# Kernel tuning notes

Hardware: AMD Instinct MI355X
Metric: run time of the kernel (lower is better)

## Reference

```python
import jax, jax.numpy as jnp
import numpy as np

N = 50000        # nodes
E = 800000       # directed edges (before self-loops)
NODE_DIM = 128
HIDDEN = 64
HEADS = 4
C = HIDDEN // HEADS   # 16 per-head channels
LAYERS = 4
G = 256          # graphs in batch
EPS = 1e-5       # BatchNorm eps
SLOPE = 0.2      # GAT leaky_relu negative slope


def setup_inputs() -> dict:
    key = jax.random.key(0)
    ks = jax.random.split(key, 12)

    def gl(k, shape, fan_in):  # glorot-ish init
        return jax.random.normal(k, shape, jnp.float32) * np.float32(1.0 / np.sqrt(fan_in))

    x = jax.random.normal(ks[0], (N, NODE_DIM), jnp.float32)
    edge_index = jax.random.randint(ks[1], (2, E), 0, N)
    batch = jnp.sort(jax.random.randint(ks[2], (N,), 0, G))

    return {
        "x": x,
        "embed_W": gl(ks[3], (NODE_DIM, HIDDEN), NODE_DIM),
        "embed_b": jnp.zeros((HIDDEN,), jnp.float32),
        "gat_W": gl(ks[4], (LAYERS, HIDDEN, HIDDEN), HIDDEN),
        "att_src": gl(ks[5], (LAYERS, HEADS, C), C),
        "att_dst": gl(ks[6], (LAYERS, HEADS, C), C),
        "gat_b": jnp.zeros((LAYERS, HIDDEN), jnp.float32),
        "bn_gamma": jnp.ones((LAYERS, HIDDEN), jnp.float32),
        "bn_beta": jnp.zeros((LAYERS, HIDDEN), jnp.float32),
        "fc1_W": gl(ks[7], (HIDDEN, HIDDEN), HIDDEN),
        "fc1_b": jnp.zeros((HIDDEN,), jnp.float32),
        "fc2_W": gl(ks[8], (HIDDEN, 1), HIDDEN),
        "fc2_b": jnp.zeros((1,), jnp.float32),
        "edge_index": edge_index,
        "batch": batch,
    }


def reference(x, embed_W, embed_b, gat_W, att_src, att_dst, gat_b,
              bn_gamma, bn_beta, fc1_W, fc1_b, fc2_W, fc2_b,
              edge_index, batch):
    # GATConv default: add self-loops (message flows src -> dst)
    loops = jnp.arange(N)
    src = jnp.concatenate([edge_index[0], loops])
    dst = jnp.concatenate([edge_index[1], loops])

    h = x @ embed_W + embed_b  # [N, HIDDEN]
    for l in range(LAYERS):
        xp = (h @ gat_W[l]).reshape(N, HEADS, C)          # per-head transform
        a_s = jnp.sum(xp * att_src[l], axis=-1)           # [N, H]
        a_d = jnp.sum(xp * att_dst[l], axis=-1)           # [N, H]
        e = jax.nn.leaky_relu(a_s[src] + a_d[dst], SLOPE) # [E', H]
        # segment softmax over incoming edges of each dst node
        m = jax.ops.segment_max(e, dst, num_segments=N)
        p = jnp.exp(e - m[dst])
        s = jax.ops.segment_sum(p, dst, num_segments=N)
        alpha = p / (s[dst] + 1e-16)                      # [E', H]
        msg = xp[src] * alpha[:, :, None]                 # [E', H, C]
        h = jax.ops.segment_sum(msg, dst, num_segments=N).reshape(N, HIDDEN) + gat_b[l]
        # BatchNorm over nodes (training-mode batch stats, biased variance)
        mu = jnp.mean(h, axis=0)
        var = jnp.var(h, axis=0)
        h = (h - mu) * jax.lax.rsqrt(var + EPS) * bn_gamma[l] + bn_beta[l]
        h = jax.nn.elu(h)

    g = jax.ops.segment_sum(h, batch, num_segments=G)     # global_add_pool
    g = jax.nn.relu(g @ fc1_W + fc1_b)                    # dropout: identity (eval)
    return (g @ fc2_W + fc2_b).reshape(-1)                # [G]
```

## Files before the change

### kernel.cpp

```cpp
#include <hip/hip_runtime.h>

#define N_NODES 50000
#define N_EDGES 800000
#define NODE_DIM 128
#define HIDDEN 64
#define HEADS 4
#define LAYERS 4
#define NGRAPH 256
#define BN_EPS 1e-5f
#define SLOPE 0.2f
#define NTILES 196
#define BN_BLOCKS 256
#define NPW 16

typedef unsigned short u16;
typedef unsigned int   u32;

__device__ __forceinline__ float b2f(u16 v) { return __uint_as_float(((u32)v) << 16); }
__device__ __forceinline__ u16 f2b(float f) {
    u32 u = __float_as_uint(f);
    u32 r = (u + 0x7FFFu + ((u >> 16) & 1u)) >> 16;
    return (u16)r;
}
__device__ __forceinline__ float ld(const void* p, int i, int isf) {
    return isf ? ((const float*)p)[i] : b2f(((const u16*)p)[i]);
}
__device__ __forceinline__ float bcast(float v, int l) {
    return __uint_as_float((u32)__builtin_amdgcn_readlane((int)__float_as_uint(v), l));
}

__global__ void k_mark(u16* out, u16 pat) { out[threadIdx.x] = pat; }

__global__ void k_init(const void* gamma, int* flag, int* cnt) {
    int i = blockIdx.x * 256 + threadIdx.x;
    if (i < N_NODES) cnt[i] = 0;
    if (i == 0) *flag = (((const u32*)gamma)[0] == 0x3F800000u) ? 1 : 0;
}

__global__ void k_count(const int* __restrict__ ei, int* __restrict__ cnt,
                        int* __restrict__ eslot) {
    int e = blockIdx.x * 256 + threadIdx.x;
    if (e >= N_EDGES) return;
    eslot[e] = atomicAdd(&cnt[ei[N_EDGES + e]], 1);
}
__global__ void k_scan1(const int* __restrict__ cnt, int* __restrict__ row_ptr,
                        int* __restrict__ tsum) {
    int b = blockIdx.x, t = threadIdx.x, i = b * 256 + t;
    int c = (i < N_NODES) ? cnt[i] : 0;
    __shared__ int ps[256];
    ps[t] = c;
    __syncthreads();
    for (int off = 1; off < 256; off <<= 1) {
        int v = (t >= off) ? ps[t - off] : 0;
        __syncthreads();
        ps[t] += v;
        __syncthreads();
    }
    if (i < N_NODES) row_ptr[i] = ps[t] - c;
    if (t == 255) tsum[b] = ps[255];
}
__global__ void k_scan3(int* __restrict__ row_ptr, const int* __restrict__ tsum) {
    __shared__ int ps[256];
    int t = threadIdx.x;
    int c = (t < NTILES) ? tsum[t] : 0;
    ps[t] = c;
    __syncthreads();
    for (int off = 1; off < 256; off <<= 1) {
        int v = (t >= off) ? ps[t - off] : 0;
        __syncthreads();
        ps[t] += v;
        __syncthreads();
    }
    int toff_b = (blockIdx.x == 0) ? 0 : ps[blockIdx.x - 1];
    int i = blockIdx.x * 256 + t;
    if (i < N_NODES) row_ptr[i] += toff_b;
    if (i == 0) row_ptr[N_NODES] = N_EDGES;
}
__global__ void k_fill(const int* __restrict__ ei, const int* __restrict__ row_ptr,
                       const int* __restrict__ eslot, int* __restrict__ col) {
    int e = blockIdx.x * 256 + threadIdx.x;
    if (e >= N_EDGES) return;
    col[row_ptr[ei[N_EDGES + e]] + eslot[e]] = ei[e];
}

template<int ISF>
__device__ __forceinline__ float2 ldx2(const void* x, int n, int t) {
    if (ISF) {
        return ((const float2*)x)[(size_t)n * (NODE_DIM / 2) + t];
    } else {
        u32 v = ((const u32*)x)[(size_t)n * (NODE_DIM / 2) + t];
        return make_float2(__uint_as_float(v << 16), __uint_as_float(v & 0xFFFF0000u));
    }
}

template<int ISF>
__device__ __forceinline__ void embed_tr_body(const void* __restrict__ x,
                                              const void* __restrict__ W,
                                              const void* __restrict__ b,
                                              const void* __restrict__ W0,
                                              const void* __restrict__ asrc,
                                              const void* __restrict__ adst,
                                              u16* __restrict__ xp16,
                                              float* __restrict__ a_s,
                                              float* __restrict__ a_d,
                                              float* __restrict__ bn_part) {
    int t = threadIdx.x;
    int n0 = blockIdx.x * NPW;
    if (blockIdx.x < BN_BLOCKS) {
        bn_part[blockIdx.x * 128 + t] = 0.f;
        bn_part[blockIdx.x * 128 + 64 + t] = 0.f;
    }
    float wreg[NODE_DIM];
#pragma unroll
    for (int k = 0; k < NODE_DIM; k++) wreg[k] = ld(W, k * HIDDEN + t, ISF);
    float w0[HIDDEN];
#pragma unroll
    for (int k = 0; k < HIDDEN; k++) w0[k] = ld(W0, k * HIDDEN + t, ISF);
    float bias = ld(b, t, ISF);
    float vsc = ld(asrc, t, ISF);
    float vdc = ld(adst, t, ISF);

    float2 r[4], rn[4];
#pragma unroll
    for (int i = 0; i < 4; i++) r[i] = ldx2<ISF>(x, n0 + i, t);

    for (int g = 0; g < NPW / 4; g++) {
        if (g + 1 < NPW / 4) {
#pragma unroll
            for (int i = 0; i < 4; i++) rn[i] = ldx2<ISF>(x, n0 + (g + 1) * 4 + i, t);
        }
#pragma unroll
        for (int i = 0; i < 4; i++) {
            int n = n0 + g * 4 + i;
            float a0 = 0.f, a1 = 0.f, a2 = 0.f, a3 = 0.f;
#pragma unroll
            for (int j = 0; j < 64; j += 2) {
                a0 = fmaf(bcast(r[i].x, j),     wreg[2 * j],     a0);
                a1 = fmaf(bcast(r[i].y, j),     wreg[2 * j + 1], a1);
                a2 = fmaf(bcast(r[i].x, j + 1), wreg[2 * j + 2], a2);
                a3 = fmaf(bcast(r[i].y, j + 1), wreg[2 * j + 3], a3);
            }
            float hv = (a0 + a1) + (a2 + a3) + bias;
            float c0 = 0.f, c1 = 0.f, c2 = 0.f, c3 = 0.f;
#pragma unroll
            for (int j = 0; j < HIDDEN; j += 4) {
                c0 = fmaf(bcast(hv, j),     w0[j],     c0);
                c1 = fmaf(bcast(hv, j + 1), w0[j + 1], c1);
                c2 = fmaf(bcast(hv, j + 2), w0[j + 2], c2);
                c3 = fmaf(bcast(hv, j + 3), w0[j + 3], c3);
            }
            float acc = (c0 + c1) + (c2 + c3);
            xp16[(size_t)n * HIDDEN + t] = f2b(acc);
            float vs = acc * vsc, vd = acc * vdc;
#pragma unroll
            for (int o = 1; o < 16; o <<= 1) {
                vs += __shfl_xor(vs, o, 16);
                vd += __shfl_xor(vd, o, 16);
            }
            if ((t & 15) == 0) {
                a_s[n * HEADS + (t >> 4)] = vs;
                a_d[n * HEADS + (t >> 4)] = vd;
            }
        }
#pragma unroll
        for (int i = 0; i < 4; i++) r[i] = rn[i];
    }
}
__global__ void __launch_bounds__(64)
k_embed_tr(const void* __restrict__ x, const void* __restrict__ W,
           const void* __restrict__ b, const void* __restrict__ W0,
           const void* __restrict__ asrc, const void* __restrict__ adst,
           const int* __restrict__ fl,
           u16* __restrict__ xp16, float* __restrict__ a_s, float* __restrict__ a_d,
           float* __restrict__ bn_part) {
    if (*fl) embed_tr_body<1>(x, W, b, W0, asrc, adst, xp16, a_s, a_d, bn_part);
    else     embed_tr_body<0>(x, W, b, W0, asrc, adst, xp16, a_s, a_d, bn_part);
}

template<int ISF>
__device__ __forceinline__ void transform_body(const float* __restrict__ h,
                                               const void* __restrict__ W,
                                               const void* __restrict__ asrc,
                                               const void* __restrict__ adst, int l,
                                               const float* __restrict__ bnss,
                                               u16* __restrict__ xp16,
                                               float* __restrict__ a_s,
                                               float* __restrict__ a_d,
                                               float* __restrict__ bn_part) {
    int t = threadIdx.x;
    int n0 = blockIdx.x * NPW;
    if (blockIdx.x < BN_BLOCKS) {
        bn_part[blockIdx.x * 128 + t] = 0.f;
        bn_part[blockIdx.x * 128 + 64 + t] = 0.f;
    }
    float wreg[HIDDEN];
#pragma unroll
    for (int k = 0; k < HIDDEN; k++) wreg[k] = ld(W, l * HIDDEN * HIDDEN + k * HIDDEN + t, ISF);
    float vsc = ld(asrc, l * HIDDEN + t, ISF);
    float vdc = ld(adst, l * HIDDEN + t, ISF);
    float sc = bnss[t], sh = bnss[64 + t];

    float v[4], vn[4];
#pragma unroll
    for (int i = 0; i < 4; i++) {
        float u = h[(size_t)(n0 + i) * HIDDEN + t];
        u = u * sc + sh;
        v[i] = u > 0.f ? u : (__expf(u) - 1.f);
    }

    for (int g = 0; g < NPW / 4; g++) {
        if (g + 1 < NPW / 4) {
#pragma unroll
            for (int i = 0; i < 4; i++)
                vn[i] = h[(size_t)(n0 + (g + 1) * 4 + i) * HIDDEN + t];
        }
#pragma unroll
        for (int i = 0; i < 4; i++) {
            int n = n0 + g * 4 + i;
            float c0 = 0.f, c1 = 0.f, c2 = 0.f, c3 = 0.f;
#pragma unroll
            for (int j = 0; j < HIDDEN; j += 4) {
                c0 = fmaf(bcast(v[i], j),     wreg[j],     c0);
                c1 = fmaf(bcast(v[i], j + 1), wreg[j + 1], c1);
                c2 = fmaf(bcast(v[i], j + 2), wreg[j + 2], c2);
                c3 = fmaf(bcast(v[i], j + 3), wreg[j + 3], c3);
            }
            float acc = (c0 + c1) + (c2 + c3);
            xp16[(size_t)n * HIDDEN + t] = f2b(acc);
            float vs = acc * vsc, vd = acc * vdc;
#pragma unroll
            for (int o = 1; o < 16; o <<= 1) {
                vs += __shfl_xor(vs, o, 16);
                vd += __shfl_xor(vd, o, 16);
            }
            if ((t & 15) == 0) {
                a_s[n * HEADS + (t >> 4)] = vs;
                a_d[n * HEADS + (t >> 4)] = vd;
            }
        }
        if (g + 1 < NPW / 4) {
#pragma unroll
            for (int i = 0; i < 4; i++) {
                float u = vn[i] * sc + sh;
                v[i] = u > 0.f ? u : (__expf(u) - 1.f);
            }
        }
    }
}
__global__ void __launch_bounds__(64)
k_transform(const float* __restrict__ h, const void* __restrict__ W,
            const void* __restrict__ asrc, const void* __restrict__ adst,
            const int* __restrict__ fl, int l,
            const float* __restrict__ bnss,
            u16* __restrict__ xp16, float* __restrict__ a_s,
            float* __restrict__ a_d, float* __restrict__ bn_part) {
    if (*fl) transform_body<1>(h, W, asrc, adst, l, bnss, xp16, a_s, a_d, bn_part);
    else     transform_body<0>(h, W, asrc, adst, l, bnss, xp16, a_s, a_d, bn_part);
}

__global__ void __launch_bounds__(256)
k_gather(const int* __restrict__ row_ptr, const int* __restrict__ col,
         const float* __restrict__ a_s, const float* __restrict__ a_d,
         const u16* __restrict__ xp16, float* __restrict__ h,
         float* __restrict__ bn_part) {
    int d = blockIdx.x * 4 + (threadIdx.x >> 6);
    int t = threadIdx.x & 63;
    int hd = t >> 4, l16 = t & 15, hb = hd << 4;
    int beg = row_ptr[d], end = row_ptr[d + 1];
    float ad = a_d[d * HEADS + hd];

    float m = a_s[d * HEADS + hd] + ad;
    m = m > 0.f ? m : SLOPE * m;
    float s = 1.f;
    float acc = b2f(xp16[(size_t)d * HIDDEN + t]);

    for (int j0 = beg; j0 < end; j0 += 16) {
        int jj = j0 + l16;
        int sv = col[jj < end ? jj : end - 1];
        float e = -1e30f;
        if (jj < end) {
            e = a_s[sv * HEADS + hd] + ad;
            e = e > 0.f ? e : SLOPE * e;
        }
        float cm = e;
#pragma unroll
        for (int o = 1; o < 16; o <<= 1) cm = fmaxf(cm, __shfl_xor(cm, o, 16));
        float nm = fmaxf(m, cm);
        float scale = __expf(m - nm);
        float alpha = (jj < end) ? __expf(e - nm) : 0.f;
        float cs = alpha;
#pragma unroll
        for (int o = 1; o < 16; o <<= 1) cs += __shfl_xor(cs, o, 16);
        s = s * scale + cs;
        acc *= scale;
#pragma unroll
        for (int q = 0; q < 16; q++) {
            int   svq = __shfl(sv, q, 64);
            float aq  = __shfl(alpha, hb + q, 64);
            acc += aq * b2f(xp16[(size_t)svq * HIDDEN + t]);
        }
        m = nm;
    }
    float v = acc / (s + 1e-16f);
    h[(size_t)d * HIDDEN + t] = v;

    __shared__ float s1[256];
    __shared__ float s2[256];
    s1[threadIdx.x] = v;
    s2[threadIdx.x] = v * v;
    __syncthreads();
    if (threadIdx.x < 64) {
        float su = s1[t] + s1[64 + t] + s1[128 + t] + s1[192 + t];
        float sq = s2[t] + s2[64 + t] + s2[128 + t] + s2[192 + t];
        float* bp = bn_part + (blockIdx.x & (BN_BLOCKS - 1)) * 128;
        atomicAdd(bp + t, su);
        atomicAdd(bp + 64 + t, sq);
    }
}

__global__ void k_bn_final(const float* __restrict__ bn_part,
                           const void* __restrict__ gamma, const void* __restrict__ beta,
                           const int* __restrict__ fl, int l, float* __restrict__ bnss) {
    int t = threadIdx.x;
    float sum = 0.f, sq = 0.f;
#pragma unroll 8
    for (int b = 0; b < BN_BLOCKS; b++) {
        sum += bn_part[b * 128 + t];
        sq  += bn_part[b * 128 + 64 + t];
    }
    int isf = *fl;
    const float inv_n = 1.f / (float)N_NODES;
    float mu  = sum * inv_n;
    float var = sq * inv_n - mu * mu;
    float sc = rsqrtf(var + BN_EPS) * ld(gamma, l * HIDDEN + t, isf);
    bnss[t]      = sc;
    bnss[64 + t] = ld(beta, l * HIDDEN + t, isf) - mu * sc;
}

__global__ void __launch_bounds__(1024)
k_poolmlp(const float* __restrict__ h, const int* __restrict__ batch,
          const float* __restrict__ bnss,
          const void* __restrict__ W1, const void* __restrict__ b1,
          const void* __restrict__ W2, const void* __restrict__ b2,
          const int* __restrict__ fl, void* __restrict__ out) {
    int gr = blockIdx.x;
    int t = threadIdx.x & 63, w = threadIdx.x >> 6;
    int lo = 0, hi = N_NODES;
    while (lo < hi) { int mid = (lo + hi) >> 1; if (batch[mid] < gr) lo = mid + 1; else hi = mid; }
    int beg = lo;
    lo = 0; hi = N_NODES;
    while (lo < hi) { int mid = (lo + hi) >> 1; if (batch[mid] < gr + 1) lo = mid + 1; else hi = mid; }
    int end = lo;
    float sc = bnss[t], sh = bnss[64 + t];
    float acc = 0.f;
    for (int n = beg + w; n < end; n += 16) {
        float v = h[(size_t)n * HIDDEN + t] * sc + sh;
        acc += v > 0.f ? v : (__expf(v) - 1.f);
    }
    __shared__ float sd[1024];
    __shared__ float gs[64];
    sd[threadIdx.x] = acc;
    __syncthreads();
    if (w < 8) sd[threadIdx.x] += sd[threadIdx.x + 512];
    __syncthreads();
    if (w < 4) sd[threadIdx.x] += sd[threadIdx.x + 256];
    __syncthreads();
    if (w < 2) sd[threadIdx.x] += sd[threadIdx.x + 128];
    __syncthreads();
    if (w == 0) gs[t] = sd[t] + sd[t + 64];
    __syncthreads();
    if (w == 0) {
        int isf = *fl;
        float a1 = ld(b1, t, isf);
        for (int k = 0; k < HIDDEN; k++) a1 += gs[k] * ld(W1, k * HIDDEN + t, isf);
        a1 = fmaxf(a1, 0.f);
        float p = a1 * ld(W2, t, isf);
#pragma unroll
        for (int o = 1; o < 64; o <<= 1) p += __shfl_xor(p, o, 64);
        if (t == 0) {
            float r = p + ld(b2, 0, isf);
            if (isf) ((float*)out)[gr] = r;
            else     ((u16*)out)[gr]   = f2b(r);
        }
    }
}

extern "C" void kernel_launch(void* const* d_in, const int* in_sizes, int n_in,
                              void* d_out, int out_size, void* d_ws, size_t ws_size,
                              hipStream_t stream) {
    u16* out16 = (u16*)d_out;

    bool sizes_ok = (n_in == 15) && (out_size == NGRAPH)
        && in_sizes[0] == N_NODES * NODE_DIM
        && in_sizes[1] == NODE_DIM * HIDDEN
        && in_sizes[2] == HIDDEN
        && in_sizes[3] == LAYERS * HIDDEN * HIDDEN
        && in_sizes[4] == LAYERS * HIDDEN
        && in_sizes[5] == LAYERS * HIDDEN
        && in_sizes[6] == LAYERS * HIDDEN
        && in_sizes[7] == LAYERS * HIDDEN
        && in_sizes[8] == LAYERS * HIDDEN
        && in_sizes[9] == HIDDEN * HIDDEN
        && in_sizes[10] == HIDDEN
        && in_sizes[11] == HIDDEN
        && in_sizes[12] == 1
        && in_sizes[13] == 2 * N_EDGES
        && in_sizes[14] == N_NODES;
    if (!sizes_ok) { k_mark<<<1, 256, 0, stream>>>(out16, 0x4442); return; }

    float* ws      = (float*)d_ws;
    float* h       = ws;
    u16*   xp16    = (u16*)(ws + 3200000);
    float* a_s     = ws + 4800000;
    float* a_d     = ws + 5000000;
    float* bn_part = ws + 5200000;
    float* bnss    = ws + 5232768;
    int* row_ptr   = (int*)(ws + 5232896);
    int* cnt       = row_ptr + 50001;
    int* eslot     = cnt + 50000;
    int* col       = eslot + 800000;
    int* tsum      = col + 800000;
    int* dflag     = tsum + 256;

    const size_t NEED_BYTES =
        (size_t)(5232896 + 50001 + 50000 + 800000 + 800000 + 256 + 1) * 4;
    if (ws_size < NEED_BYTES) { k_mark<<<1, 256, 0, stream>>>(out16, 0x447A); return; }

    const void* x        = d_in[0];
    const void* embed_W  = d_in[1];
    const void* embed_b  = d_in[2];
    const void* gat_W    = d_in[3];
    const void* att_src  = d_in[4];
    const void* att_dst  = d_in[5];
    const void* bn_gamma = d_in[7];
    const void* bn_beta  = d_in[8];
    const void* fc1_W    = d_in[9];
    const void* fc1_b    = d_in[10];
    const void* fc2_W    = d_in[11];
    const void* fc2_b    = d_in[12];
    const int* ei        = (const int*)d_in[13];
    const int* batch     = (const int*)d_in[14];

    const int e_blocks = (N_EDGES + 255) / 256;
    k_init<<<(N_NODES + 255) / 256, 256, 0, stream>>>(bn_gamma, dflag, cnt);
    k_count<<<e_blocks, 256, 0, stream>>>(ei, cnt, eslot);
    k_scan1<<<NTILES, 256, 0, stream>>>(cnt, row_ptr, tsum);
    k_scan3<<<NTILES, 256, 0, stream>>>(row_ptr, tsum);
    k_fill<<<e_blocks, 256, 0, stream>>>(ei, row_ptr, eslot, col);

    k_embed_tr<<<N_NODES / NPW, 64, 0, stream>>>(x, embed_W, embed_b, gat_W,
                                                 att_src, att_dst, dflag,
                                                 xp16, a_s, a_d, bn_part);

    for (int l = 0; l < LAYERS; l++) {
        if (l > 0)
            k_transform<<<N_NODES / NPW, 64, 0, stream>>>(h, gat_W, att_src, att_dst,
                                                          dflag, l, bnss,
                                                          xp16, a_s, a_d, bn_part);
        k_gather<<<N_NODES / 4, 256, 0, stream>>>(row_ptr, col, a_s, a_d, xp16, h, bn_part);
        k_bn_final<<<1, 64, 0, stream>>>(bn_part, bn_gamma, bn_beta, dflag, l, bnss);
    }

    k_poolmlp<<<NGRAPH, 1024, 0, stream>>>(h, batch, bnss, fc1_W, fc1_b, fc2_W, fc2_b,
                                           dflag, d_out);
}
```

Measured before the change: 471.0 us.

## Fold embed and first GAT weights; stage node rows in LDS for transforms

A setup kernel now precomputes embed_W·gat_W[0] and the folded bias, so the first transform is a single 128→64 matvec instead of two chained matvecs. Both transform kernels replace per-lane readlane broadcasts with per-wave double-buffered LDS rows read as float4. They also launch 256-thread blocks holding four independent waves instead of 64-thread blocks. This is meant to cut ALU and scalar-broadcast work in the dense transforms, at the cost of LDS traffic, a small extra precompute, and slightly different rounding.

```diff
diff --git a/kernel.cpp b/kernel.cpp
--- a/kernel.cpp
+++ b/kernel.cpp
@@ -12,6 +12,7 @@
 #define NTILES 196
 #define BN_BLOCKS 256
 #define NPW 16
+#define GBLK ((N_NODES + 4 * NPW - 1) / (4 * NPW))
 
 typedef unsigned short u16;
 typedef unsigned int   u32;
@@ -25,16 +26,33 @@
 __device__ __forceinline__ float ld(const void* p, int i, int isf) {
     return isf ? ((const float*)p)[i] : b2f(((const u16*)p)[i]);
 }
-__device__ __forceinline__ float bcast(float v, int l) {
-    return __uint_as_float((u32)__builtin_amdgcn_readlane((int)__float_as_uint(v), l));
-}
 
 __global__ void k_mark(u16* out, u16 pat) { out[threadIdx.x] = pat; }
 
-__global__ void k_init(const void* gamma, int* flag, int* cnt) {
-    int i = blockIdx.x * 256 + threadIdx.x;
-    if (i < N_NODES) cnt[i] = 0;
-    if (i == 0) *flag = (((const u32*)gamma)[0] == 0x3F800000u) ? 1 : 0;
+__global__ void k_initw(const void* gamma, const void* We, const void* b,
+                        const void* gatW, int* flag, int* cnt,
+                        float* __restrict__ Wf, float* __restrict__ bf) {
+    int isf = (((const u32*)gamma)[0] == 0x3F800000u) ? 1 : 0;
+    if (blockIdx.x < NTILES) {
+        int i = blockIdx.x * 256 + threadIdx.x;
+        if (i < N_NODES) cnt[i] = 0;
+        if (i == 0) *flag = isf;
+    } else {
+        int r = blockIdx.x - NTILES;
+        int c = threadIdx.x;
+        if (c < HIDDEN) {
+            float acc = 0.f;
+            if (r < NODE_DIM) {
+                for (int k = 0; k < HIDDEN; k++)
+                    acc += ld(We, r * HIDDEN + k, isf) * ld(gatW, k * HIDDEN + c, isf);
+                Wf[r * HIDDEN + c] = acc;
+            } else {
+                for (int k = 0; k < HIDDEN; k++)
+                    acc += ld(b, k, isf) * ld(gatW, k * HIDDEN + c, isf);
+                bf[c] = acc;
+            }
+        }
+    }
 }
 
 __global__ void k_count(const int* __restrict__ ei, int* __restrict__ cnt,
@@ -94,35 +112,30 @@
 }
 
 template<int ISF>
-__device__ __forceinline__ void embed_tr_body(const void* __restrict__ x,
-                                              const void* __restrict__ W,
-                                              const void* __restrict__ b,
-                                              const void* __restrict__ W0,
-                                              const void* __restrict__ asrc,
-                                              const void* __restrict__ adst,
-                                              u16* __restrict__ xp16,
-                                              float* __restrict__ a_s,
-                                              float* __restrict__ a_d,
-                                              float* __restrict__ bn_part) {
-    int t = threadIdx.x;
-    int n0 = blockIdx.x * NPW;
-    if (blockIdx.x < BN_BLOCKS) {
-        bn_part[blockIdx.x * 128 + t] = 0.f;
-        bn_part[blockIdx.x * 128 + 64 + t] = 0.f;
-    }
+__device__ __forceinline__ void xform0_body(const void* __restrict__ x,
+                                            const float* __restrict__ Wf,
+                                            const float* __restrict__ bf,
+                                            const void* __restrict__ asrc,
+                                            const void* __restrict__ adst,
+                                            u16* __restrict__ xp16,
+                                            float* __restrict__ a_s,
+                                            float* __restrict__ a_d) {
+    int w = threadIdx.x >> 6, t = threadIdx.x & 63;
+    int n0 = blockIdx.x * (4 * NPW) + w * NPW;
+    if (n0 >= N_NODES) return;
+    __shared__ float xs[4][2][4][NODE_DIM];
     float wreg[NODE_DIM];
 #pragma unroll
-    for (int k = 0; k < NODE_DIM; k++) wreg[k] = ld(W, k * HIDDEN + t, ISF);
-    float w0[HIDDEN];
-#pragma unroll
-    for (int k = 0; k < HIDDEN; k++) w0[k] = ld(W0, k * HIDDEN + t, ISF);
-    float bias = ld(b, t, ISF);
+    for (int k = 0; k < NODE_DIM; k++) wreg[k] = Wf[k * HIDDEN + t];
+    float bias = bf[t];
     float vsc = ld(asrc, t, ISF);
     float vdc = ld(adst, t, ISF);
 
     float2 r[4], rn[4];
 #pragma unroll
     for (int i = 0; i < 4; i++) r[i] = ldx2<ISF>(x, n0 + i, t);
+#pragma unroll
+    for (int i = 0; i < 4; i++) *(float2*)&xs[w][0][i][2 * t] = r[i];
 
     for (int g = 0; g < NPW / 4; g++) {
         if (g + 1 < NPW / 4) {
@@ -132,24 +145,17 @@
 #pragma unroll
         for (int i = 0; i < 4; i++) {
             int n = n0 + g * 4 + i;
+            const float* xr = xs[w][g & 1][i];
             float a0 = 0.f, a1 = 0.f, a2 = 0.f, a3 = 0.f;
 #pragma unroll
-            for (int j = 0; j < 64; j += 2) {
-                a0 = fmaf(bcast(r[i].x, j),     wreg[2 * j],     a0);
-                a1 = fmaf(bcast(r[i].y, j),     wreg[2 * j + 1], a1);
-                a2 = fmaf(bcast(r[i].x, j + 1), wreg[2 * j + 2], a2);
-                a3 = fmaf(bcast(r[i].y, j + 1), wreg[2 * j + 3], a3);
-            }
-            float hv = (a0 + a1) + (a2 + a3) + bias;
-            float c0 = 0.f, c1 = 0.f, c2 = 0.f, c3 = 0.f;
-#pragma unroll
-            for (int j = 0; j < HIDDEN; j += 4) {
-                c0 = fmaf(bcast(hv, j),     w0[j],     c0);
-                c1 = fmaf(bcast(hv, j + 1), w0[j + 1], c1);
-                c2 = fmaf(bcast(hv, j + 2), w0[j + 2], c2);
-                c3 = fmaf(bcast(hv, j + 3), w0[j + 3], c3);
-            }
-            float acc = (c0 + c1) + (c2 + c3);
+            for (int k = 0; k < NODE_DIM; k += 4) {
+                float4 xv = *(const float4*)&xr[k];
+                a0 += xv.x * wreg[k];
+                a1 += xv.y * wreg[k + 1];
+                a2 += xv.z * wreg[k + 2];
+                a3 += xv.w * wreg[k + 3];
+            }
+            float acc = (a0 + a1) + (a2 + a3) + bias;
             xp16[(size_t)n * HIDDEN + t] = f2b(acc);
             float vs = acc * vsc, vd = acc * vdc;
 #pragma unroll
@@ -162,19 +168,23 @@
                 a_d[n * HEADS + (t >> 4)] = vd;
             }
         }
-#pragma unroll
-        for (int i = 0; i < 4; i++) r[i] = rn[i];
-    }
-}
-__global__ void __launch_bounds__(64)
-k_embed_tr(const void* __restrict__ x, const void* __restrict__ W,
-           const void* __restrict__ b, const void* __restrict__ W0,
-           const void* __restrict__ asrc, const void* __restrict__ adst,
-           const int* __restrict__ fl,
-           u16* __restrict__ xp16, float* __restrict__ a_s, float* __restrict__ a_d,
-           float* __restrict__ bn_part) {
-    if (*fl) embed_tr_body<1>(x, W, b, W0, asrc, adst, xp16, a_s, a_d, bn_part);
-    else     embed_tr_body<0>(x, W, b, W0, asrc, adst, xp16, a_s, a_d, bn_part);
+        if (g + 1 < NPW / 4) {
+#pragma unroll
+            for (int i = 0; i < 4; i++) *(float2*)&xs[w][(g + 1) & 1][i][2 * t] = rn[i];
+        }
+    }
+}
+__global__ void __launch_bounds__(256)
+k_xform0(const void* __restrict__ x, const float* __restrict__ Wf,
+         const float* __restrict__ bf,
+         const void* __restrict__ asrc, const void* __restrict__ adst,
+         const int* __restrict__ fl,
+         u16* __restrict__ xp16, float* __restrict__ a_s, float* __restrict__ a_d,
+         float* __restrict__ bn_part) {
+    if (blockIdx.x < BN_BLOCKS && threadIdx.x < 128)
+        bn_part[blockIdx.x * 128 + threadIdx.x] = 0.f;
+    if (*fl) xform0_body<1>(x, Wf, bf, asrc, adst, xp16, a_s, a_d);
+    else     xform0_body<0>(x, Wf, bf, asrc, adst, xp16, a_s, a_d);
 }
 
 template<int ISF>
@@ -185,14 +195,11 @@
                                                const float* __restrict__ bnss,
                                                u16* __restrict__ xp16,
                                                float* __restrict__ a_s,
-                                               float* __restrict__ a_d,
-                                               float* __restrict__ bn_part) {
-    int t = threadIdx.x;
-    int n0 = blockIdx.x * NPW;
-    if (blockIdx.x < BN_BLOCKS) {
-        bn_part[blockIdx.x * 128 + t] = 0.f;
-        bn_part[blockIdx.x * 128 + 64 + t] = 0.f;
-    }
+                                               float* __restrict__ a_d) {
+    int w = threadIdx.x >> 6, t = threadIdx.x & 63;
+    int n0 = blockIdx.x * (4 * NPW) + w * NPW;
+    if (n0 >= N_NODES) return;
+    __shared__ float hsb[4][2][4][HIDDEN];
     float wreg[HIDDEN];
 #pragma unroll
     for (int k = 0; k < HIDDEN; k++) wreg[k] = ld(W, l * HIDDEN * HIDDEN + k * HIDDEN + t, ISF);
@@ -200,30 +207,34 @@
     float vdc = ld(adst, l * HIDDEN + t, ISF);
     float sc = bnss[t], sh = bnss[64 + t];
 
-    float v[4], vn[4];
+    float r[4], rn[4];
 #pragma unroll
     for (int i = 0; i < 4; i++) {
         float u = h[(size_t)(n0 + i) * HIDDEN + t];
         u = u * sc + sh;
-        v[i] = u > 0.f ? u : (__expf(u) - 1.f);
-    }
+        r[i] = u > 0.f ? u : (__expf(u) - 1.f);
+    }
+#pragma unroll
+    for (int i = 0; i < 4; i++) hsb[w][0][i][t] = r[i];
 
     for (int g = 0; g < NPW / 4; g++) {
         if (g + 1 < NPW / 4) {
 #pragma unroll
             for (int i = 0; i < 4; i++)
-                vn[i] = h[(size_t)(n0 + (g + 1) * 4 + i) * HIDDEN + t];
+                rn[i] = h[(size_t)(n0 + (g + 1) * 4 + i) * HIDDEN + t];
         }
 #pragma unroll
         for (int i = 0; i < 4; i++) {
             int n = n0 + g * 4 + i;
+            const float* hr = hsb[w][g & 1][i];
             float c0 = 0.f, c1 = 0.f, c2 = 0.f, c3 = 0.f;
 #pragma unroll
-            for (int j = 0; j < HIDDEN; j += 4) {
-                c0 = fmaf(bcast(v[i], j),     wreg[j],     c0);
-                c1 = fmaf(bcast(v[i], j + 1), wreg[j + 1], c1);
-                c2 = fmaf(bcast(v[i], j + 2), wreg[j + 2], c2);
-                c3 = fmaf(bcast(v[i], j + 3), wreg[j + 3], c3);
+            for (int k = 0; k < HIDDEN; k += 4) {
+                float4 xv = *(const float4*)&hr[k];
+                c0 += xv.x * wreg[k];
+                c1 += xv.y * wreg[k + 1];
+                c2 += xv.z * wreg[k + 2];
+                c3 += xv.w * wreg[k + 3];
             }
             float acc = (c0 + c1) + (c2 + c3);
             xp16[(size_t)n * HIDDEN + t] = f2b(acc);
@@ -241,21 +252,23 @@
         if (g + 1 < NPW / 4) {
 #pragma unroll
             for (int i = 0; i < 4; i++) {
-                float u = vn[i] * sc + sh;
-                v[i] = u > 0.f ? u : (__expf(u) - 1.f);
-            }
-        }
-    }
-}
-__global__ void __launch_bounds__(64)
+                float u = rn[i] * sc + sh;
+                hsb[w][(g + 1) & 1][i][t] = u > 0.f ? u : (__expf(u) - 1.f);
+            }
+        }
+    }
+}
+__global__ void __launch_bounds__(256)
 k_transform(const float* __restrict__ h, const void* __restrict__ W,
             const void* __restrict__ asrc, const void* __restrict__ adst,
             const int* __restrict__ fl, int l,
             const float* __restrict__ bnss,
             u16* __restrict__ xp16, float* __restrict__ a_s,
             float* __restrict__ a_d, float* __restrict__ bn_part) {
-    if (*fl) transform_body<1>(h, W, asrc, adst, l, bnss, xp16, a_s, a_d, bn_part);
-    else     transform_body<0>(h, W, asrc, adst, l, bnss, xp16, a_s, a_d, bn_part);
+    if (blockIdx.x < BN_BLOCKS && threadIdx.x < 128)
+        bn_part[blockIdx.x * 128 + threadIdx.x] = 0.f;
+    if (*fl) transform_body<1>(h, W, asrc, adst, l, bnss, xp16, a_s, a_d);
+    else     transform_body<0>(h, W, asrc, adst, l, bnss, xp16, a_s, a_d);
 }
 
 __global__ void __launch_bounds__(256)
@@ -421,9 +434,12 @@
     int* col       = eslot + 800000;
     int* tsum      = col + 800000;
     int* dflag     = tsum + 256;
+    float* Wf      = (float*)(dflag + 1);
+    float* bf      = Wf + NODE_DIM * HIDDEN;
 
     const size_t NEED_BYTES =
-        (size_t)(5232896 + 50001 + 50000 + 800000 + 800000 + 256 + 1) * 4;
+        (size_t)(5232896 + 50001 + 50000 + 800000 + 800000 + 256 + 1
+                 + NODE_DIM * HIDDEN + HIDDEN) * 4;
     if (ws_size < NEED_BYTES) { k_mark<<<1, 256, 0, stream>>>(out16, 0x447A); return; }
 
     const void* x        = d_in[0];
@@ -442,21 +458,21 @@
     const int* batch     = (const int*)d_in[14];
 
     const int e_blocks = (N_EDGES + 255) / 256;
-    k_init<<<(N_NODES + 255) / 256, 256, 0, stream>>>(bn_gamma, dflag, cnt);
+    k_initw<<<NTILES + NODE_DIM + 1, 256, 0, stream>>>(bn_gamma, embed_W, embed_b,
+                                                       gat_W, dflag, cnt, Wf, bf);
     k_count<<<e_blocks, 256, 0, stream>>>(ei, cnt, eslot);
     k_scan1<<<NTILES, 256, 0, stream>>>(cnt, row_ptr, tsum);
     k_scan3<<<NTILES, 256, 0, stream>>>(row_ptr, tsum);
     k_fill<<<e_blocks, 256, 0, stream>>>(ei, row_ptr, eslot, col);
 
-    k_embed_tr<<<N_NODES / NPW, 64, 0, stream>>>(x, embed_W, embed_b, gat_W,
-                                                 att_src, att_dst, dflag,
-                                                 xp16, a_s, a_d, bn_part);
+    k_xform0<<<GBLK, 256, 0, stream>>>(x, Wf, bf, att_src, att_dst, dflag,
+                                       xp16, a_s, a_d, bn_part);
 
     for (int l = 0; l < LAYERS; l++) {
         if (l > 0)
-            k_transform<<<N_NODES / NPW, 64, 0, stream>>>(h, gat_W, att_src, att_dst,
-                                                          dflag, l, bnss,
-                                                          xp16, a_s, a_d, bn_part);
+            k_transform<<<GBLK, 256, 0, stream>>>(h, gat_W, att_src, att_dst,
+                                                  dflag, l, bnss,
+                                                  xp16, a_s, a_d, bn_part);
         k_gather<<<N_NODES / 4, 256, 0, stream>>>(row_ptr, col, a_s, a_d, xp16, h, bn_part);
         k_bn_final<<<1, 64, 0, stream>>>(bn_part, bn_gamma, bn_beta, dflag, l, bnss);
     }
```

After: 466.8 us. No clear change (-0.9%).
